# Optimization experiments

Hardware: AMD Instinct MI355X
Metric: run time of the kernel (lower is better)

The kernel has to match this reference:

```python
import jax, jax.numpy as jnp
import numpy as np

N_NODES = 100000
N_EDGES = 1600000
N_GRAPHS = 512
BN_EPS = 1e-5


def setup_inputs() -> dict:
    key = jax.random.key(0)
    ks = jax.random.split(key, 16)
    x = jax.random.normal(ks[0], (N_NODES, 66), dtype=jnp.float32)
    edge_index = jax.random.randint(ks[1], (2, N_EDGES), 0, N_NODES, dtype=jnp.int64)
    edge_attr = jax.random.normal(ks[2], (N_EDGES, 1), dtype=jnp.float32)
    batch = jnp.sort(jax.random.randint(ks[3], (N_NODES,), 0, N_GRAPHS, dtype=jnp.int64))
    def glorot(k, shape):
        lim = np.sqrt(6.0 / (shape[0] + shape[1]))
        return jax.random.uniform(k, shape, jnp.float32, -lim, lim)
    return {
        "x": x, "edge_index": edge_index, "edge_attr": edge_attr, "batch": batch,
        "W1": glorot(ks[4], (66, 64)), "b1": jnp.zeros((64,), jnp.float32),
        "g1": jnp.ones((64,), jnp.float32), "be1": jnp.zeros((64,), jnp.float32),
        "W2": glorot(ks[5], (64, 32)), "b2": jnp.zeros((32,), jnp.float32),
        "g2": jnp.ones((32,), jnp.float32), "be2": jnp.zeros((32,), jnp.float32),
        "Wm1": glorot(ks[6], (64, 32)), "bm1": jnp.zeros((32,), jnp.float32),
        "Wm2": glorot(ks[7], (32, 2)), "bm2": jnp.zeros((2,), jnp.float32),
    }


def gcn_conv(x, W, b, src, dst, n_nodes):
    # PyG GCNConv: add self-loops, symmetric D^-1/2 (A+I) D^-1/2 normalization.
    xw = x @ W                                             # [N, F]
    deg = jnp.zeros((n_nodes,), xw.dtype).at[dst].add(1.0) + 1.0  # incl. self-loop
    dinv = jax.lax.rsqrt(deg)                              # deg^-1/2
    coef = dinv[src] * dinv[dst]                           # [E]
    agg = jnp.zeros_like(xw).at[dst].add(xw[src] * coef[:, None])
    agg = agg + xw * (dinv * dinv)[:, None]                # self-loop messages
    return agg + b


def batch_norm(x, gamma, beta):
    # training-mode BN over the node dimension (reference is deterministic)
    mu = jnp.mean(x, axis=0)
    var = jnp.mean(jnp.square(x - mu), axis=0)
    return gamma * (x - mu) * jax.lax.rsqrt(var + BN_EPS) + beta


def reference(x, edge_index, edge_attr, batch,
              W1, b1, g1, be1, W2, b2, g2, be2, Wm1, bm1, Wm2, bm2):
    src, dst = edge_index[0], edge_index[1]
    h = x[:, :66]
    h = jax.nn.elu(batch_norm(gcn_conv(h, W1, b1, src, dst, N_NODES), g1, be1))
    # dropout omitted (eval-mode reference)
    h = jax.nn.elu(batch_norm(gcn_conv(h, W2, b2, src, dst, N_NODES), g2, be2))
    counts = jax.ops.segment_sum(jnp.ones((N_NODES,), h.dtype), batch, num_segments=N_GRAPHS)
    mean_pool = jax.ops.segment_sum(h, batch, num_segments=N_GRAPHS) / jnp.maximum(counts, 1.0)[:, None]
    max_pool = jax.ops.segment_max(h, batch, num_segments=N_GRAPHS)
    max_pool = jnp.where(counts[:, None] > 0, max_pool, 0.0)
    g = jnp.concatenate([mean_pool, max_pool], axis=1)     # [G, 64]
    g = jax.nn.elu(g @ Wm1 + bm1)
    return g @ Wm2 + bm2                                   # [G, num_classes]
```

## Files before the change

kernel.cpp:

```cpp
#include <hip/hip_runtime.h>
#include <math.h>

constexpr int NN = 100000;
constexpr int NE = 1600000;
constexpr int NG = 512;
constexpr int NBKT = (NN + 127) / 128;
constexpr int BSTR = 2560;
constexpr int PADREG = BSTR + 896;
constexpr int BCAP = 3072;

typedef unsigned short bf16_t;
typedef unsigned int u32x4 __attribute__((ext_vector_type(4)));
__device__ __forceinline__ bf16_t f2bf(float f) {
    unsigned u = __float_as_uint(f);
    unsigned r = (u + 0x7fffu + ((u >> 16) & 1u)) >> 16;
    return (bf16_t)r;
}
__device__ __forceinline__ float bflo(unsigned u) { return __uint_as_float(u << 16); }
__device__ __forceinline__ float bfhi(unsigned u) { return __uint_as_float(u & 0xffff0000u); }
__device__ __forceinline__ unsigned bfpack(float lo, float hi) {
    return ((unsigned)f2bf(hi) << 16) | (unsigned)f2bf(lo);
}
__device__ __forceinline__ float eluf(float x) {
    return x > 0.f ? x : expm1f(x);
}

__global__ __launch_bounds__(1024) void k_scatter_bkt(const int* __restrict__ src,
                                                      const int* __restrict__ dst,
                                                      int* __restrict__ bktCur,
                                                      int* __restrict__ ebuf) {
    __shared__ int cnt[NBKT];
    __shared__ int base[NBKT];
    int tid = threadIdx.x;
    for (int i = tid; i < NBKT; i += 1024) cnt[i] = 0;
    __syncthreads();
    int per = (NE + gridDim.x - 1) / gridDim.x;
    int e0 = blockIdx.x * per;
    int e1 = min(e0 + per, NE);
    for (int e = e0 + tid; e < e1; e += 1024) {
        int d = __builtin_nontemporal_load(dst + e);
        atomicAdd(&cnt[d >> 7], 1);
    }
    __syncthreads();
    for (int i = tid; i < NBKT; i += 1024) {
        int c = cnt[i];
        base[i] = i * BSTR + (c ? atomicAdd(&bktCur[i], c) : 0);
        cnt[i] = 0;
    }
    __syncthreads();
    for (int e = e0 + tid; e < e1; e += 1024) {
        int s = __builtin_nontemporal_load(src + e);
        int d = __builtin_nontemporal_load(dst + e);
        int b = d >> 7;
        int off = atomicAdd(&cnt[b], 1);
        ebuf[base[b] + off] = (s << 7) | (d & 127);
    }
}

__global__ __launch_bounds__(256) void k_bktsort(const int* __restrict__ bktCur,
                                                 const int* __restrict__ ebuf,
                                                 int* __restrict__ csr,
                                                 int2* __restrict__ rowInfo,
                                                 float* __restrict__ dinv,
                                                 const int* __restrict__ batch,
                                                 int* __restrict__ gptr) {
    int b = blockIdx.x, tid = threadIdx.x;
    if (b == NBKT) {
        for (int g = tid; g <= NG; g += 256) {
            if (g == NG) { gptr[NG] = NN; continue; }
            int lo = 0, hi = NN;
            while (lo < hi) {
                int mid = (lo + hi) >> 1;
                if (batch[mid] < g) lo = mid + 1; else hi = mid;
            }
            gptr[g] = lo;
        }
        return;
    }
    __shared__ int sbuf[BCAP];
    __shared__ int cnt[128], scn[128], cur[128];
    __shared__ int padTotS;
    int base = b * BSTR;
    int n = min(bktCur[b], BSTR);
    int pbase = b * PADREG;
    for (int i = tid; i < n; i += 256) sbuf[i] = __builtin_nontemporal_load(ebuf + base + i);
    if (tid < 128) cnt[tid] = 0;
    __syncthreads();
    for (int i = tid; i < n; i += 256) atomicAdd(&cnt[sbuf[i] & 127], 1);
    __syncthreads();
    int deg = (tid < 128) ? cnt[tid] : 0;
    int pcnt = (deg + 7) & ~7;
    if (tid < 128) scn[tid] = pcnt;
    __syncthreads();
    for (int off = 1; off < 128; off <<= 1) {
        int t = (tid < 128 && tid >= off) ? scn[tid - off] : 0;
        __syncthreads();
        if (tid < 128) scn[tid] += t;
        __syncthreads();
    }
    if (tid == 127) padTotS = scn[127];
    if (tid < 128) {
        int ex = scn[tid] - pcnt;
        cur[tid] = ex;
        int node = b * 128 + tid;
        if (node < NN) {
            rowInfo[node] = make_int2(pbase + ex, pbase + ex + pcnt);
            dinv[node] = rsqrtf((float)deg + 1.0f);
        }
    }
    __syncthreads();
    int padTot = padTotS;
    for (int i = tid; i < padTot; i += 256) csr[pbase + i] = NN;
    __syncthreads();
    for (int i = tid; i < n; i += 256) {
        int p = sbuf[i];
        int pos = atomicAdd(&cur[p & 127], 1);
        csr[pbase + pos] = p >> 7;
    }
}

__global__ void k_gemm1(const float* __restrict__ x, const float* __restrict__ W1,
                        const float* __restrict__ dinv, bf16_t* __restrict__ y1b) {
    __shared__ __align__(16) float sx[64 * 68];
    __shared__ __align__(16) float sw[66 * 64];
    int tid = threadIdx.x;
    for (int i = tid; i < 66 * 32; i += 256) ((float2*)sw)[i] = ((const float2*)W1)[i];
    int base = blockIdx.x * 64;
    int rows = min(64, NN - base);
    int cnt2v = rows * 33;
    const float2* xp = (const float2*)(x + base * 66);
    for (int i = tid; i < cnt2v; i += 256) {
        int r = i / 33, kk = i - r * 33;
        ((float2*)(sx + r * 68))[kk] = xp[i];
    }
    __syncthreads();
    int tr = tid >> 4, tc = tid & 15;
    const float* sxr = sx + tr * 4 * 68;
    const float* swc = sw + tc * 4;
    float acc[4][4];
#pragma unroll
    for (int r = 0; r < 4; ++r)
#pragma unroll
        for (int c = 0; c < 4; ++c) acc[r][c] = 0.f;
#pragma unroll 4
    for (int ks = 0; ks < 64; ks += 4) {
        float4 a0 = *(const float4*)(sxr + 0 * 68 + ks);
        float4 a1 = *(const float4*)(sxr + 1 * 68 + ks);
        float4 a2 = *(const float4*)(sxr + 2 * 68 + ks);
        float4 a3 = *(const float4*)(sxr + 3 * 68 + ks);
        float4 b0 = *(const float4*)(swc + (ks + 0) * 64);
        float4 b1 = *(const float4*)(swc + (ks + 1) * 64);
        float4 b2 = *(const float4*)(swc + (ks + 2) * 64);
        float4 b3 = *(const float4*)(swc + (ks + 3) * 64);
#define FMA4(ar, bv, kk) do { \
        acc[0][0] = fmaf(a0.ar, bv.x, acc[0][0]); acc[0][1] = fmaf(a0.ar, bv.y, acc[0][1]); \
        acc[0][2] = fmaf(a0.ar, bv.z, acc[0][2]); acc[0][3] = fmaf(a0.ar, bv.w, acc[0][3]); \
        acc[1][0] = fmaf(a1.ar, bv.x, acc[1][0]); acc[1][1] = fmaf(a1.ar, bv.y, acc[1][1]); \
        acc[1][2] = fmaf(a1.ar, bv.z, acc[1][2]); acc[1][3] = fmaf(a1.ar, bv.w, acc[1][3]); \
        acc[2][0] = fmaf(a2.ar, bv.x, acc[2][0]); acc[2][1] = fmaf(a2.ar, bv.y, acc[2][1]); \
        acc[2][2] = fmaf(a2.ar, bv.z, acc[2][2]); acc[2][3] = fmaf(a2.ar, bv.w, acc[2][3]); \
        acc[3][0] = fmaf(a3.ar, bv.x, acc[3][0]); acc[3][1] = fmaf(a3.ar, bv.y, acc[3][1]); \
        acc[3][2] = fmaf(a3.ar, bv.z, acc[3][2]); acc[3][3] = fmaf(a3.ar, bv.w, acc[3][3]); } while (0)
        FMA4(x, b0, 0); FMA4(y, b1, 1); FMA4(z, b2, 2); FMA4(w, b3, 3);
#undef FMA4
    }
#pragma unroll
    for (int k = 64; k < 66; ++k) {
        float4 bt = *(const float4*)(swc + k * 64);
#pragma unroll
        for (int r = 0; r < 4; ++r) {
            float av = sxr[r * 68 + k];
            acc[r][0] = fmaf(av, bt.x, acc[r][0]);
            acc[r][1] = fmaf(av, bt.y, acc[r][1]);
            acc[r][2] = fmaf(av, bt.z, acc[r][2]);
            acc[r][3] = fmaf(av, bt.w, acc[r][3]);
        }
    }
    bf16_t* dstp = y1b + (tc >> 2) * ((NN + 1) * 16) + (tc & 3) * 4;
#pragma unroll
    for (int r = 0; r < 4; ++r) {
        int nn = base + tr * 4 + r;
        if (nn < NN) {
            float di = dinv[nn];
            ushort4 o;
            o.x = f2bf(di * acc[r][0]); o.y = f2bf(di * acc[r][1]);
            o.z = f2bf(di * acc[r][2]); o.w = f2bf(di * acc[r][3]);
            *(ushort4*)(dstp + (size_t)nn * 16) = o;
        } else if (nn == NN) {
            ushort4 o; o.x = 0; o.y = 0; o.z = 0; o.w = 0;
            *(ushort4*)(dstp + (size_t)nn * 16) = o;
        }
    }
}

template<int NSL>
__global__ __launch_bounds__(256) void k_gather(const int2* __restrict__ rowInfo,
                                                const int* __restrict__ csr,
                                                const float* __restrict__ dinv,
                                                const uint4* __restrict__ yb,
                                                uint4* __restrict__ aggb,
                                                float* __restrict__ sums,
                                                float* __restrict__ sqs) {
    constexpr int SH = (NSL == 4) ? 2 : 1;
    __shared__ float sSum[16], sSq[16];
    int tid = threadIdx.x;
    if (tid < 16) { sSum[tid] = 0.f; sSq[tid] = 0.f; }
    __syncthreads();
    int slice = blockIdx.x & (NSL - 1);
    int part = blockIdx.x >> SH;
    int nparts = gridDim.x >> SH;
    int lane = tid & 1;
    int grp = tid >> 1;
    const uint4* y = yb + (size_t)slice * ((NN + 1) * 2) + lane;
    uint4* agg = aggb + (size_t)slice * (NN * 2) + lane;
    float s[8], q[8];
#pragma unroll
    for (int k = 0; k < 8; ++k) { s[k] = 0.f; q[k] = 0.f; }
    for (int n = part * 128 + grp; n < NN; n += nparts * 128) {
        int2 ri = rowInfo[n];
        float a[8];
#pragma unroll
        for (int k = 0; k < 8; ++k) a[k] = 0.f;
        int j = ri.x;
        unsigned long long c0 = 0, c1 = 0, c2 = 0, c3 = 0;
        if (j < ri.y) {
            const unsigned long long* cp = (const unsigned long long*)(csr + j);
            c0 = cp[0]; c1 = cp[1]; c2 = cp[2]; c3 = cp[3];
        }
        while (j < ri.y) {
            int i0 = (int)(c0 & 0xffffffffu), i1 = (int)(c0 >> 32);
            int i2 = (int)(c1 & 0xffffffffu), i3 = (int)(c1 >> 32);
            int i4 = (int)(c2 & 0xffffffffu), i5 = (int)(c2 >> 32);
            int i6 = (int)(c3 & 0xffffffffu), i7 = (int)(c3 >> 32);
            j += 8;
            uint4 v0 = y[i0 * 2];
            uint4 v1 = y[i1 * 2];
            uint4 v2 = y[i2 * 2];
            uint4 v3 = y[i3 * 2];
            uint4 v4 = y[i4 * 2];
            uint4 v5 = y[i5 * 2];
            uint4 v6 = y[i6 * 2];
            uint4 v7 = y[i7 * 2];
            if (j < ri.y) {
                const unsigned long long* np = (const unsigned long long*)(csr + j);
                c0 = np[0]; c1 = np[1]; c2 = np[2]; c3 = np[3];
            }
#define ACC8(v) do { \
            a[0] += bflo((v).x); a[1] += bfhi((v).x); \
            a[2] += bflo((v).y); a[3] += bfhi((v).y); \
            a[4] += bflo((v).z); a[5] += bfhi((v).z); \
            a[6] += bflo((v).w); a[7] += bfhi((v).w); } while (0)
            ACC8(v0); ACC8(v1); ACC8(v2); ACC8(v3);
            ACC8(v4); ACC8(v5); ACC8(v6); ACC8(v7);
#undef ACC8
        }
        uint4 vs = y[n * 2];
        float di = dinv[n];
        a[0] = di * (a[0] + bflo(vs.x)); a[1] = di * (a[1] + bfhi(vs.x));
        a[2] = di * (a[2] + bflo(vs.y)); a[3] = di * (a[3] + bfhi(vs.y));
        a[4] = di * (a[4] + bflo(vs.z)); a[5] = di * (a[5] + bfhi(vs.z));
        a[6] = di * (a[6] + bflo(vs.w)); a[7] = di * (a[7] + bfhi(vs.w));
        u32x4 o;
        o.x = bfpack(a[0], a[1]); o.y = bfpack(a[2], a[3]);
        o.z = bfpack(a[4], a[5]); o.w = bfpack(a[6], a[7]);
        __builtin_nontemporal_store(o, (u32x4*)(agg + n * 2));
#pragma unroll
        for (int k = 0; k < 8; ++k) {
            float av = (k == 0) ? a[0] : (k == 1) ? a[1] : (k == 2) ? a[2] : (k == 3) ? a[3]
                     : (k == 4) ? a[4] : (k == 5) ? a[5] : (k == 6) ? a[6] : a[7];
            s[k] += av; q[k] += av * av;
        }
    }
#pragma unroll
    for (int k = 0; k < 8; ++k) {
        float sv = s[k], qv = q[k];
#pragma unroll
        for (int off = 2; off < 64; off <<= 1) {
            sv += __shfl_xor(sv, off);
            qv += __shfl_xor(qv, off);
        }
        if ((tid & 63) < 2) {
            atomicAdd(&sSum[lane * 8 + k], sv);
            atomicAdd(&sSq[lane * 8 + k], qv);
        }
    }
    __syncthreads();
    if (tid < 16) {
        unsafeAtomicAdd(&sums[slice * 16 + tid], sSum[tid]);
        unsafeAtomicAdd(&sqs[slice * 16 + tid], sSq[tid]);
    }
}

__global__ void k_bn_gemm2(const unsigned* __restrict__ agg1b, const float* __restrict__ sums,
                           const float* __restrict__ sqs, const float* __restrict__ gamma,
                           const float* __restrict__ beta, const float* __restrict__ W2,
                           const float* __restrict__ dinv, bf16_t* __restrict__ y2b) {
    __shared__ float sh[8 * 64];
    __shared__ float sW[64 * 32];
    __shared__ float sscale[64], sshift[64];
    int tid = threadIdx.x;
    if (tid < 64) {
        float mu = sums[tid] * (1.0f / NN);
        float var = sqs[tid] * (1.0f / NN) - mu * mu;
        float sc = gamma[tid] * rsqrtf(var + 1e-5f);
        sscale[tid] = sc;
        sshift[tid] = beta[tid] - mu * sc;
    }
#pragma unroll
    for (int i = tid; i < 64 * 32; i += 256) sW[i] = W2[i];
    __syncthreads();
    int base = blockIdx.x * 8;
    {
        int r = tid >> 5, q = tid & 31;
        int slice = q >> 3, lane = q & 7;
        int n = base + r;
        int col = slice * 16 + lane * 2;
        float v0 = 0.f, v1 = 0.f;
        if (n < NN) {
            unsigned u = agg1b[(size_t)slice * NN * 8 + n * 8 + lane];
            v0 = eluf(fmaf(bflo(u), sscale[col], sshift[col]));
            v1 = eluf(fmaf(bfhi(u), sscale[col + 1], sshift[col + 1]));
        }
        sh[r * 64 + col] = v0;
        sh[r * 64 + col + 1] = v1;
    }
    __syncthreads();
    int r = tid >> 5, c = tid & 31;
    int n = base + r;
    bf16_t* dstp = y2b + (c >> 4) * ((NN + 1) * 16) + (c & 15);
    if (n < NN) {
        float acc = 0.f;
#pragma unroll
        for (int k = 0; k < 64; ++k) acc = fmaf(sh[r * 64 + k], sW[k * 32 + c], acc);
        dstp[n * 16] = f2bf(dinv[n] * acc);
    } else if (n == NN) {
        dstp[n * 16] = 0;
    }
}

__global__ void k_poolmlp(const unsigned* __restrict__ agg2b, const float* __restrict__ sums,
                          const float* __restrict__ sqs, const float* __restrict__ gamma,
                          const float* __restrict__ beta, const int* __restrict__ gptr,
                          const float* __restrict__ Wm1, const float* __restrict__ bm1,
                          const float* __restrict__ Wm2, const float* __restrict__ bm2,
                          float* __restrict__ out) {
    __shared__ float sscale[32], sshift[32];
    __shared__ float red[256];
    __shared__ float gr[64];
    __shared__ float h[32];
    int tid = threadIdx.x;
    if (tid < 32) {
        float mu = sums[tid] * (1.0f / NN);
        float var = sqs[tid] * (1.0f / NN) - mu * mu;
        float sc = gamma[tid] * rsqrtf(var + 1e-5f);
        sscale[tid] = sc;
        sshift[tid] = beta[tid] - mu * sc;
    }
    __syncthreads();
    int g = blockIdx.x;
    int c = tid & 31, r = tid >> 5;
    int beg = gptr[g], end = gptr[g + 1];
    float scl = sscale[c], shf = sshift[c];
    const unsigned* ap = agg2b + (size_t)(c >> 4) * NN * 8 + ((c >> 1) & 7);
    bool hi = (c & 1);
    float s = 0.f, m = -INFINITY;
    for (int n = beg + r; n < end; n += 8) {
        unsigned u = ap[n * 8];
        float v = eluf(fmaf(hi ? bfhi(u) : bflo(u), scl, shf));
        s += v;
        m = fmaxf(m, v);
    }
    red[tid] = s;
    __syncthreads();
    int cnt = end - beg;
    if (r == 0) {
        float stot = 0.f;
#pragma unroll
        for (int i = 0; i < 8; ++i) stot += red[i * 32 + c];
        gr[c] = stot / fmaxf((float)cnt, 1.f);
    }
    __syncthreads();
    red[tid] = m;
    __syncthreads();
    if (r == 0) {
        float mtot = -INFINITY;
#pragma unroll
        for (int i = 0; i < 8; ++i) mtot = fmaxf(mtot, red[i * 32 + c]);
        gr[32 + c] = (cnt > 0) ? mtot : 0.f;
    }
    __syncthreads();
    if (tid < 32) {
        float acc = bm1[tid];
#pragma unroll
        for (int k = 0; k < 64; ++k) acc = fmaf(gr[k], Wm1[k * 32 + tid], acc);
        h[tid] = eluf(acc);
    }
    __syncthreads();
    if (tid < 2) {
        float acc = bm2[tid];
#pragma unroll
        for (int k = 0; k < 32; ++k) acc = fmaf(h[k], Wm2[k * 2 + tid], acc);
        out[g * 2 + tid] = acc;
    }
}

extern "C" void kernel_launch(void* const* d_in, const int* in_sizes, int n_in,
                              void* d_out, int out_size, void* d_ws, size_t ws_size,
                              hipStream_t stream) {
    const float* x    = (const float*)d_in[0];
    const int*   eidx = (const int*)d_in[1];
    const int*   src  = eidx;
    const int*   dst  = eidx + NE;
    const int*   batch = (const int*)d_in[3];
    const float* W1  = (const float*)d_in[4];
    const float* g1  = (const float*)d_in[6];
    const float* be1 = (const float*)d_in[7];
    const float* W2  = (const float*)d_in[8];
    const float* g2  = (const float*)d_in[10];
    const float* be2 = (const float*)d_in[11];
    const float* Wm1 = (const float*)d_in[12];
    const float* bm1 = (const float*)d_in[13];
    const float* Wm2 = (const float*)d_in[14];
    const float* bm2 = (const float*)d_in[15];
    float* out = (float*)d_out;

    constexpr int CSRSZ = NBKT * PADREG + 16;
    int*    bktCur  = (int*)d_ws;
    float*  S       = (float*)(bktCur + 800);
    int*    gptr    = (int*)(S + 512);
    int*    csr     = gptr + 544;
    int2*   rowInfo = (int2*)(csr + CSRSZ);
    float*  dinv    = (float*)(rowInfo + 100000);
    bf16_t* y1b     = (bf16_t*)(dinv + 100000);
    bf16_t* agg1b   = y1b + (NN + 1) * 64;
    bf16_t* y2b     = agg1b + NN * 64;
    bf16_t* agg2b   = y2b + (NN + 1) * 32;
    int*    ebuf    = (int*)y2b;

    float* sum1 = S;        float* sq1 = S + 64;
    float* sum2 = S + 128;  float* sq2 = S + 160;

    (void)hipMemsetAsync(bktCur, 0, (800 + 512) * sizeof(int), stream);

    k_scatter_bkt<<<512, 1024, 0, stream>>>(src, dst, bktCur, ebuf);
    k_bktsort<<<NBKT + 1, 256, 0, stream>>>(bktCur, ebuf, csr, rowInfo, dinv, batch, gptr);

    k_gemm1<<<(NN + 63) / 64, 256, 0, stream>>>(x, W1, dinv, y1b);
    k_gather<4><<<3128, 256, 0, stream>>>(rowInfo, csr, dinv,
                                          (const uint4*)y1b, (uint4*)agg1b,
                                          sum1, sq1);

    k_bn_gemm2<<<NN / 8 + 1, 256, 0, stream>>>((const unsigned*)agg1b, sum1, sq1,
                                               g1, be1, W2, dinv, y2b);
    k_gather<2><<<1564, 256, 0, stream>>>(rowInfo, csr, dinv,
                                          (const uint4*)y2b, (uint4*)agg2b,
                                          sum2, sq2);

    k_poolmlp<<<NG, 256, 0, stream>>>((const unsigned*)agg2b, sum2, sq2, g2, be2, gptr,
                                      Wm1, bm1, Wm2, bm2, out);
}
```

Measured before the change: 289.0 us.

## Split CSR index loads across lane pairs and enlarge row tile in BN-GEMM2

In the gather kernel, each pair of lanes that shares a node now loads half of the 8 neighbor indices with one 16-byte load and exchanges them through shuffles, instead of both lanes loading all 32 bytes. This halves redundant index traffic but adds shuffle and select instructions. In k_bn_gemm2, each block now processes 32 rows instead of 8, which amortizes the W2 staging into shared memory. W2 is stored transposed with padding so the dot product can use float4 LDS reads.

```diff
diff --git a/kernel.cpp b/kernel.cpp
--- a/kernel.cpp
+++ b/kernel.cpp
@@ -222,12 +222,20 @@
 #pragma unroll
         for (int k = 0; k < 8; ++k) a[k] = 0.f;
         int j = ri.x;
-        unsigned long long c0 = 0, c1 = 0, c2 = 0, c3 = 0;
+        unsigned long long mh0 = 0, mh1 = 0;
         if (j < ri.y) {
-            const unsigned long long* cp = (const unsigned long long*)(csr + j);
-            c0 = cp[0]; c1 = cp[1]; c2 = cp[2]; c3 = cp[3];
+            const uint4* cp4 = (const uint4*)(csr + j);
+            uint4 h = cp4[lane];
+            mh0 = ((unsigned long long)h.y << 32) | h.x;
+            mh1 = ((unsigned long long)h.w << 32) | h.z;
         }
         while (j < ri.y) {
+            unsigned long long p0 = __shfl_xor(mh0, 1);
+            unsigned long long p1 = __shfl_xor(mh1, 1);
+            unsigned long long c0 = lane ? p0 : mh0;
+            unsigned long long c1 = lane ? p1 : mh1;
+            unsigned long long c2 = lane ? mh0 : p0;
+            unsigned long long c3 = lane ? mh1 : p1;
             int i0 = (int)(c0 & 0xffffffffu), i1 = (int)(c0 >> 32);
             int i2 = (int)(c1 & 0xffffffffu), i3 = (int)(c1 >> 32);
             int i4 = (int)(c2 & 0xffffffffu), i5 = (int)(c2 >> 32);
@@ -242,8 +250,10 @@
             uint4 v6 = y[i6 * 2];
             uint4 v7 = y[i7 * 2];
             if (j < ri.y) {
-                const unsigned long long* np = (const unsigned long long*)(csr + j);
-                c0 = np[0]; c1 = np[1]; c2 = np[2]; c3 = np[3];
+                const uint4* np = (const uint4*)(csr + j);
+                uint4 h = np[lane];
+                mh0 = ((unsigned long long)h.y << 32) | h.x;
+                mh1 = ((unsigned long long)h.w << 32) | h.z;
             }
 #define ACC8(v) do { \
             a[0] += bflo((v).x); a[1] += bfhi((v).x); \
@@ -295,8 +305,9 @@
                            const float* __restrict__ sqs, const float* __restrict__ gamma,
                            const float* __restrict__ beta, const float* __restrict__ W2,
                            const float* __restrict__ dinv, bf16_t* __restrict__ y2b) {
-    __shared__ float sh[8 * 64];
-    __shared__ float sW[64 * 32];
+    constexpr int RB = 32;
+    __shared__ __align__(16) float sh[RB * 64];
+    __shared__ __align__(16) float sWt[32 * 68];
     __shared__ float sscale[64], sshift[64];
     int tid = threadIdx.x;
     if (tid < 64) {
@@ -307,17 +318,21 @@
         sshift[tid] = beta[tid] - mu * sc;
     }
 #pragma unroll
-    for (int i = tid; i < 64 * 32; i += 256) sW[i] = W2[i];
-    __syncthreads();
-    int base = blockIdx.x * 8;
-    {
-        int r = tid >> 5, q = tid & 31;
-        int slice = q >> 3, lane = q & 7;
+    for (int i = tid; i < 64 * 32; i += 256) {
+        int k = i >> 5, c = i & 31;
+        sWt[c * 68 + k] = W2[i];
+    }
+    __syncthreads();
+    int base = blockIdx.x * RB;
+#pragma unroll
+    for (int rr = 0; rr < RB / 8; ++rr) {
+        int r = (tid >> 5) + rr * 8, qq = tid & 31;
+        int slice = qq >> 3, lane = qq & 7;
         int n = base + r;
         int col = slice * 16 + lane * 2;
         float v0 = 0.f, v1 = 0.f;
         if (n < NN) {
-            unsigned u = agg1b[(size_t)slice * NN * 8 + n * 8 + lane];
+            unsigned u = agg1b[(size_t)slice * NN * 8 + (size_t)n * 8 + lane];
             v0 = eluf(fmaf(bflo(u), sscale[col], sshift[col]));
             v1 = eluf(fmaf(bfhi(u), sscale[col + 1], sshift[col + 1]));
         }
@@ -325,16 +340,29 @@
         sh[r * 64 + col + 1] = v1;
     }
     __syncthreads();
-    int r = tid >> 5, c = tid & 31;
-    int n = base + r;
+    int c = tid & 31;
     bf16_t* dstp = y2b + (c >> 4) * ((NN + 1) * 16) + (c & 15);
-    if (n < NN) {
-        float acc = 0.f;
-#pragma unroll
-        for (int k = 0; k < 64; ++k) acc = fmaf(sh[r * 64 + k], sW[k * 32 + c], acc);
-        dstp[n * 16] = f2bf(dinv[n] * acc);
-    } else if (n == NN) {
-        dstp[n * 16] = 0;
+    const float* swr = sWt + c * 68;
+#pragma unroll
+    for (int rr = 0; rr < RB / 8; ++rr) {
+        int r = (tid >> 5) + rr * 8;
+        int n = base + r;
+        if (n < NN) {
+            const float* shr = sh + r * 64;
+            float acc = 0.f;
+#pragma unroll
+            for (int k4 = 0; k4 < 64; k4 += 4) {
+                float4 av = *(const float4*)(shr + k4);
+                float4 bv = *(const float4*)(swr + k4);
+                acc = fmaf(av.x, bv.x, acc);
+                acc = fmaf(av.y, bv.y, acc);
+                acc = fmaf(av.z, bv.z, acc);
+                acc = fmaf(av.w, bv.w, acc);
+            }
+            dstp[(size_t)n * 16] = f2bf(dinv[n] * acc);
+        } else if (n == NN) {
+            dstp[(size_t)NN * 16] = 0;
+        }
     }
 }
 
@@ -450,8 +478,8 @@
                                           (const uint4*)y1b, (uint4*)agg1b,
                                           sum1, sq1);
 
-    k_bn_gemm2<<<NN / 8 + 1, 256, 0, stream>>>((const unsigned*)agg1b, sum1, sq1,
-                                               g1, be1, W2, dinv, y2b);
+    k_bn_gemm2<<<NN / 32 + 1, 256, 0, stream>>>((const unsigned*)agg1b, sum1, sq1,
+                                                g1, be1, W2, dinv, y2b);
     k_gather<2><<<1564, 256, 0, stream>>>(rowInfo, csr, dinv,
                                           (const uint4*)y2b, (uint4*)agg2b,
                                           sum2, sq2);
```

Result: no change. 284.1 us (-1.7%).
